# Performance work log

Measured on AMD Instinct MI355X. Metric: run time of the kernel, lower is better.

The kernel has to match this reference:

```python
import jax, jax.numpy as jnp
import numpy as np
from jax import lax

B, T, I, H, O = 64, 1024, 128, 512, 10
TAU_MIN, TAU_MAX = 5.0, 50.0


def setup_inputs() -> dict:
    key = jax.random.key(0)
    ks = jax.random.split(key, 12)
    s = lambda fan_in: 1.0 / np.sqrt(fan_in)
    x = jax.random.normal(ks[0], (B, T, I), dtype=jnp.float32)
    W_in = jax.random.normal(ks[1], (I, H), dtype=jnp.float32) * s(I)
    b_in = jnp.zeros((H,), dtype=jnp.float32)
    # recurrent weight, scaled down to mimic spectral-radius 0.9 init
    W_rec = jax.random.normal(ks[2], (H, H), dtype=jnp.float32) * (0.9 / np.sqrt(H))
    bias = jnp.zeros((H,), dtype=jnp.float32)
    W_tau1 = jax.random.normal(ks[3], (2 * H, H // 2), dtype=jnp.float32) * s(2 * H)
    b_tau1 = jnp.zeros((H // 2,), dtype=jnp.float32)
    W_tau2 = jax.random.normal(ks[4], (H // 2, H), dtype=jnp.float32) * s(H // 2)
    b_tau2 = jnp.zeros((H,), dtype=jnp.float32)
    W_out = jax.random.normal(ks[5], (H, O), dtype=jnp.float32) * s(H)
    b_out = jnp.zeros((O,), dtype=jnp.float32)
    return {"x": x, "W_in": W_in, "b_in": b_in, "W_rec": W_rec, "bias": bias,
            "W_tau1": W_tau1, "b_tau1": b_tau1, "W_tau2": W_tau2, "b_tau2": b_tau2,
            "W_out": W_out, "b_out": b_out}


def reference(x, W_in, b_in, W_rec, bias, W_tau1, b_tau1, W_tau2, b_tau2, W_out, b_out):
    # Input projection precomputed for all timesteps: [B, T, H]
    xp = jnp.einsum('bti,ih->bth', x, W_in) + b_in

    def step(h, xt):
        # tau adapter MLP: sigmoid(relu(cat(x,h) W1 + b1) W2 + b2)
        ctx = jnp.concatenate([xt, h], axis=-1)          # [B, 2H]
        tau_scale = jax.nn.sigmoid(jax.nn.relu(ctx @ W_tau1 + b_tau1) @ W_tau2 + b_tau2)
        tau = TAU_MIN + tau_scale * (TAU_MAX - TAU_MIN)  # [B, H]
        drive = jnp.tanh(xt + h @ W_rec.T + bias)
        new_h = h + (-h + drive) / tau                   # Euler step, dt = 1
        return new_h, new_h

    h0 = jnp.zeros((x.shape[0], W_rec.shape[0]), dtype=x.dtype)
    _, hs = lax.scan(step, h0, jnp.swapaxes(xp, 0, 1))   # [T, B, H]
    hs = jnp.swapaxes(hs, 0, 1)                          # [B, T, H]
    return hs @ W_out + b_out                            # [B, T, O]
```

## Files before the change

### kernel.cpp

```cpp
#include <hip/hip_runtime.h>
#include <hip/hip_fp16.h>
#include <math.h>

#define Bsz 64
#define Tsz 1024
#define Isz 128
#define Hsz 512
#define KH  256
#define Osz 10

__global__ __launch_bounds__(256) void gemm_bias_kernel(
    const float* __restrict__ A, const float* __restrict__ Bw,
    const float* __restrict__ bias, float* __restrict__ C,
    int M, int N, int K)
{
  __shared__ float As[32][68];
  const int tid = threadIdx.x;
  const int m0 = blockIdx.x * 64;
  const int n0 = blockIdx.y * 128;
  const int ty = tid >> 5, tx = tid & 31;

  float acc[8][4] = {{0.f}};

  for (int kk = 0; kk < K; kk += 32) {
    __syncthreads();
#pragma unroll
    for (int i = tid; i < 64 * 32; i += 256) {
      int m = i >> 5, k = i & 31;
      As[k][m] = A[(size_t)(m0 + m) * K + kk + k];
    }
    __syncthreads();
#pragma unroll
    for (int k = 0; k < 32; ++k) {
      const float4 bv = *(const float4*)(&Bw[(size_t)(kk + k) * N + n0 + tx * 4]);
      float a[8];
#pragma unroll
      for (int i = 0; i < 8; ++i) a[i] = As[k][ty * 8 + i];
#pragma unroll
      for (int i = 0; i < 8; ++i) {
        acc[i][0] = fmaf(a[i], bv.x, acc[i][0]);
        acc[i][1] = fmaf(a[i], bv.y, acc[i][1]);
        acc[i][2] = fmaf(a[i], bv.z, acc[i][2]);
        acc[i][3] = fmaf(a[i], bv.w, acc[i][3]);
      }
    }
  }

  const float4 bb = *(const float4*)(&bias[n0 + tx * 4]);
#pragma unroll
  for (int i = 0; i < 8; ++i) {
    float4 v;
    v.x = acc[i][0] + bb.x; v.y = acc[i][1] + bb.y;
    v.z = acc[i][2] + bb.z; v.w = acc[i][3] + bb.w;
    *(float4*)(&C[(size_t)(m0 + ty * 8 + i) * N + n0 + tx * 4]) = v;
  }
}

__global__ __launch_bounds__(256) void wc_kernel(
    const float* __restrict__ W_in, const float* __restrict__ W1a,
    float* __restrict__ Wc)
{
  __shared__ float row[Hsz];
  const int i = blockIdx.x, c = threadIdx.x;
  for (int h = c; h < Hsz; h += 256) row[h] = W_in[(size_t)i * Hsz + h];
  __syncthreads();
  float acc = 0.f;
#pragma unroll 8
  for (int h = 0; h < Hsz; ++h)
    acc = fmaf(row[h], W1a[(size_t)h * KH + c], acc);
  Wc[(size_t)i * KH + c] = acc;
}

__global__ __launch_bounds__(256) void bu_kernel(
    const float* __restrict__ b_in, const float* __restrict__ W1a,
    const float* __restrict__ b_tau1, float* __restrict__ bU)
{
  const int c = threadIdx.x;
  float acc = b_tau1[c];
#pragma unroll 8
  for (int h = 0; h < Hsz; ++h)
    acc = fmaf(b_in[h], W1a[(size_t)h * KH + c], acc);
  bU[c] = acc;
}

__device__ __forceinline__ int dot4i8(int a, int b, int acc) {
#if __has_builtin(__builtin_amdgcn_sdot4)
  return __builtin_amdgcn_sdot4(a, b, acc, false);
#else
  acc += ((a << 24) >> 24) * ((b << 24) >> 24);
  acc += ((a << 16) >> 24) * ((b << 16) >> 24);
  acc += ((a << 8)  >> 24) * ((b << 8)  >> 24);
  acc += (a >> 24) * (b >> 24);
  return acc;
#endif
}


__global__ __launch_bounds__(256) void drive_scale_kernel(
    const float* __restrict__ W_rec, float* __restrict__ CS0)
{
  const int j = blockIdx.x * 256 + threadIdx.x;
  float m = 0.f;
  for (int k = 0; k < Hsz; ++k)
    m = fmaxf(m, fabsf(W_rec[(size_t)j * Hsz + k]));
  CS0[j] = m;
}

__global__ __launch_bounds__(256) void drive_quant_kernel(
    const float* __restrict__ W_rec, const float* __restrict__ CS0,
    unsigned* __restrict__ Q0)
{
  int i = blockIdx.x * 256 + threadIdx.x;
  if (i >= 32 * Hsz * 4) return;
  int di = i & 3, j = (i >> 2) & 511, g = i >> 11;
  int k0 = 16 * g + 4 * di;
  float ma = CS0[j];
  float r = (ma > 0.f) ? (127.f / ma) : 0.f;
  unsigned out = 0;
#pragma unroll
  for (int e = 0; e < 4; ++e) {
    int q = __float2int_rn(W_rec[(size_t)j * Hsz + k0 + e] * r);
    out |= ((unsigned)(q & 255)) << (8 * e);
  }
  Q0[i] = out;
}

__global__ __launch_bounds__(256) void tau1_scale_kernel(
    const float* __restrict__ W1b, float* __restrict__ CS1)
{
  const int c = threadIdx.x;
  float m = 0.f;
  for (int j = 0; j < Hsz; ++j)
    m = fmaxf(m, fabsf(W1b[(size_t)j * KH + c]));
  CS1[c] = m;
}

__global__ __launch_bounds__(256) void tau1_quant_kernel(
    const float* __restrict__ W1b, const float* __restrict__ CS1,
    unsigned* __restrict__ Q1)
{
  int i = blockIdx.x * 256 + threadIdx.x;
  if (i >= 32 * KH * 4) return;
  int di = i & 3, c = (i >> 2) & 255, g = i >> 10;
  int j0 = 16 * g + 4 * di;
  float ma = CS1[c];
  float r = (ma > 0.f) ? (127.f / ma) : 0.f;
  unsigned out = 0;
#pragma unroll
  for (int e = 0; e < 4; ++e) {
    int q = __float2int_rn(W1b[(size_t)(j0 + e) * KH + c] * r);
    out |= ((unsigned)(q & 255)) << (8 * e);
  }
  Q1[i] = out;
}

__global__ __launch_bounds__(256) void tau2_scale_kernel(
    const float* __restrict__ W_tau2, float* __restrict__ CS2)
{
  const int j = blockIdx.x * 256 + threadIdx.x;
  float m = 0.f;
  for (int k = 0; k < KH; ++k)
    m = fmaxf(m, fabsf(W_tau2[(size_t)k * Hsz + j]));
  CS2[j] = m;
}

__global__ __launch_bounds__(256) void tau2_quant_kernel(
    const float* __restrict__ W_tau2, const float* __restrict__ CS2,
    unsigned* __restrict__ Q2)
{
  int i = blockIdx.x * 256 + threadIdx.x;
  if (i >= 16 * Hsz * 4) return;
  int di = i & 3, j = (i >> 2) & 511, g = i >> 11;
  int k0 = 16 * g + 4 * di;
  float ma = CS2[j];
  float r = (ma > 0.f) ? (127.f / ma) : 0.f;
  unsigned out = 0;
#pragma unroll
  for (int e = 0; e < 4; ++e) {
    int q = __float2int_rn(W_tau2[(size_t)(k0 + e) * Hsz + j] * r);
    out |= ((unsigned)(q & 255)) << (8 * e);
  }
  Q2[i] = out;
}

__global__ __launch_bounds__(512) void scan_kernel(
    float* __restrict__ xps,
    const float* __restrict__ U,
    const unsigned* __restrict__ Q0,
    const unsigned* __restrict__ Q1,
    const unsigned* __restrict__ Q2,
    const float* __restrict__ CS0,
    const float* __restrict__ CS1,
    const float* __restrict__ CS2,
    const float* __restrict__ bias,
    const float* __restrict__ b_tau2)
{
  const int b = blockIdx.x;
  const int tid = threadIdx.x;
  const int hs = tid >> 8;
  const int c  = tid & 255;

  extern __shared__ __align__(16) uint4 Wlds[];
  __shared__ __align__(16) int Hq[2][128];
  __shared__ __align__(16) unsigned char Aq[KH];
  __shared__ float scaleA[4];
  __shared__ int parti[2][KH];

  const float bias_r = bias[tid];
  const float bt2_r  = b_tau2[tid];
  const float cs0r = CS0[tid] * (1.0f / 16129.0f);
  const float csr  = CS1[c]   * (1.0f / 16129.0f);
  const float cs2r = CS2[tid] * (1.0f / 16129.0f);
  float hold = 0.f;
  if (tid < 128) { Hq[0][tid] = 0; Hq[1][tid] = 0; }

  float* xprow = xps + (size_t)b * Tsz * Hsz;
  const float* Urow = U + (size_t)b * Tsz * KH;

  const uint4* __restrict__ q0 = (const uint4*)Q0 + tid;
  const uint4* __restrict__ q1 = (const uint4*)Q1 + (size_t)(hs * 16) * 256 + c;
  const uint4* __restrict__ q2 = (const uint4*)Q2 + tid;
  const uint4* Aq4 = (const uint4*)Aq;

#pragma unroll
  for (int i = 0; i < 16; ++i)
    Wlds[i * 512 + tid] = q2[(size_t)i * 512];
#pragma unroll
  for (int i = 0; i < 2; ++i)
    Wlds[8192 + i * 512 + tid] = q0[(size_t)(30 + i) * 512];

  uint4 w0r[28];
#pragma unroll
  for (int g = 0; g < 28; ++g) w0r[g] = q0[(size_t)g * 512];
  uint4 w1r[16];
#pragma unroll
  for (int g = 0; g < 16; ++g) w1r[g] = q1[(size_t)g * 256];

  __syncthreads();

  float xpv = xprow[tid];
  float Uv  = (tid < KH) ? Urow[tid] : 0.f;

  for (int t = 0; t < Tsz; ++t) {
    const uint4* h4 = (const uint4*)Hq[t & 1];

    int a0 = 0, a1 = 0;
#pragma unroll
    for (int g = 0; g < 16; ++g) {
      const uint4 w  = w1r[g];
      const uint4 hv = h4[hs * 16 + g];
      a0 = dot4i8((int)w.x, (int)hv.x, a0); a1 = dot4i8((int)w.y, (int)hv.y, a1);
      a0 = dot4i8((int)w.z, (int)hv.z, a0); a1 = dot4i8((int)w.w, (int)hv.w, a1);
    }
    parti[hs][c] = a0 + a1;
    __syncthreads();

    if (tid < KH) {
      float aval = fmaxf(Uv + (float)(parti[0][tid] + parti[1][tid]) * csr, 0.f);
      float m = aval;
#pragma unroll
      for (int off = 32; off >= 1; off >>= 1)
        m = fmaxf(m, __shfl_xor(m, off));
      if ((tid & 63) == 0) scaleA[tid >> 6] = m;
      const float r = (m > 0.f) ? (127.f / m) : 0.f;
      Aq[tid] = (unsigned char)__float2int_rn(aval * r);
    }
    __syncthreads();

    const float xpn = xprow[Hsz + tid];
    const float Un  = (tid < KH) ? Urow[KH + tid] : 0.f;

    int d0i = 0, d1i = 0;
    int t2a0 = 0, t2a1 = 0;
    float s = bt2_r;
#pragma unroll
    for (int g = 0; g < 16; ++g) {
      uint4 w0, w1;
      if (g < 14) {
        w0 = w0r[2 * g];
        w1 = w0r[2 * g + 1];
      } else if (g == 14) {
        w0 = q0[(size_t)28 * 512];
        w1 = q0[(size_t)29 * 512];
      } else {
        w0 = Wlds[8192 + tid];
        w1 = Wlds[8192 + 512 + tid];
      }
      const uint4 hv0 = h4[2 * g], hv1 = h4[2 * g + 1];
      d0i = dot4i8((int)w0.x, (int)hv0.x, d0i); d1i = dot4i8((int)w0.y, (int)hv0.y, d1i);
      d0i = dot4i8((int)w0.z, (int)hv0.z, d0i); d1i = dot4i8((int)w0.w, (int)hv0.w, d1i);
      d0i = dot4i8((int)w1.x, (int)hv1.x, d0i); d1i = dot4i8((int)w1.y, (int)hv1.y, d1i);
      d0i = dot4i8((int)w1.z, (int)hv1.z, d0i); d1i = dot4i8((int)w1.w, (int)hv1.w, d1i);

      const uint4 wt = Wlds[g * 512 + tid];
      const uint4 av = Aq4[g];
      t2a0 = dot4i8((int)wt.x, (int)av.x, t2a0); t2a1 = dot4i8((int)wt.y, (int)av.y, t2a1);
      t2a0 = dot4i8((int)wt.z, (int)av.z, t2a0); t2a1 = dot4i8((int)wt.w, (int)av.w, t2a1);
      if ((g & 3) == 3) {
        s += (float)(t2a0 + t2a1) * cs2r * scaleA[g >> 2];
        t2a0 = 0; t2a1 = 0;
      }
    }

    const float d = xpv + bias_r + (float)(d0i + d1i) * cs0r;
    const float tau = 5.0f + 45.0f / (1.0f + __expf(-s));
    const float e2 = __expf(2.0f * d);
    const float drv = 1.0f - 2.0f / (e2 + 1.0f);
    const float hnew = hold + (drv - hold) / tau;
    hold = hnew;
    ((char*)Hq[(t + 1) & 1])[tid] = (char)(__float2int_rn(hnew * 127.f) & 255);
    xprow[tid] = hnew;
    __syncthreads();

    xpv = xpn; Uv = Un;
    xprow += Hsz;
    Urow  += KH;
  }
}

__global__ __launch_bounds__(256) void outproj_kernel(
    const float* __restrict__ hs, const float* __restrict__ W_out,
    const float* __restrict__ b_out, float* __restrict__ out)
{
  __shared__ float hsL[16][516];
  __shared__ float WL[Hsz * Osz];
  const int tid = threadIdx.x;
  const size_t m0 = (size_t)blockIdx.x * 16;

  for (int i = tid; i < Hsz * Osz; i += 256) WL[i] = W_out[i];

  const float4* src = (const float4*)(hs + m0 * Hsz);
#pragma unroll
  for (int i = 0; i < 8; ++i) {
    int idx = i * 256 + tid;
    *(float4*)&hsL[idx >> 7][(idx & 127) * 4] = src[idx];
  }
  __syncthreads();

  const int r = tid >> 4, o = tid & 15;
  if (o < Osz) {
    float acc = b_out[o];
#pragma unroll 8
    for (int k4 = 0; k4 < 128; ++k4) {
      const float4 h4 = *(const float4*)&hsL[r][k4 * 4];
      acc = fmaf(h4.x, WL[(4 * k4 + 0) * Osz + o], acc);
      acc = fmaf(h4.y, WL[(4 * k4 + 1) * Osz + o], acc);
      acc = fmaf(h4.z, WL[(4 * k4 + 2) * Osz + o], acc);
      acc = fmaf(h4.w, WL[(4 * k4 + 3) * Osz + o], acc);
    }
    out[(m0 + r) * Osz + o] = acc;
  }
}

extern "C" void kernel_launch(void* const* d_in, const int* in_sizes, int n_in,
                              void* d_out, int out_size, void* d_ws, size_t ws_size,
                              hipStream_t stream) {
  (void)in_sizes; (void)n_in; (void)out_size; (void)ws_size;

  const float* x      = (const float*)d_in[0];
  const float* W_in   = (const float*)d_in[1];
  const float* b_in   = (const float*)d_in[2];
  const float* W_rec  = (const float*)d_in[3];
  const float* bias   = (const float*)d_in[4];
  const float* W_tau1 = (const float*)d_in[5];
  const float* b_tau1 = (const float*)d_in[6];
  const float* W_tau2 = (const float*)d_in[7];
  const float* b_tau2 = (const float*)d_in[8];
  const float* W_out  = (const float*)d_in[9];
  const float* b_out  = (const float*)d_in[10];
  float* out = (float*)d_out;

  char* ws = (char*)d_ws;
  size_t off = 0;
  float* xps = (float*)(ws + off); off += (size_t)Bsz * Tsz * Hsz * 4;
  float* U   = (float*)(ws + off); off += (size_t)Bsz * Tsz * KH * 4;
  unsigned* Q0 = (unsigned*)(ws + off); off += (size_t)32 * Hsz * 4 * 4;
  unsigned* Q1 = (unsigned*)(ws + off); off += (size_t)32 * KH  * 4 * 4;
  unsigned* Q2 = (unsigned*)(ws + off); off += (size_t)16 * Hsz * 4 * 4;
  float* CS0   = (float*)(ws + off); off += 512 * 4;
  float* CS1   = (float*)(ws + off); off += 256 * 4;
  float* CS2   = (float*)(ws + off); off += 512 * 4;
  float* Wc    = (float*)(ws + off); off += (size_t)Isz * KH * 4;
  float* bU    = (float*)(ws + off); off += 256 * 4;

  const float* W1a = W_tau1;
  const float* W1b = W_tau1 + (size_t)Hsz * KH;

  const int M = Bsz * Tsz;

  (void)hipFuncSetAttribute((const void*)scan_kernel,
                            hipFuncAttributeMaxDynamicSharedMemorySize, 147456);

  drive_scale_kernel<<<2, 256, 0, stream>>>(W_rec, CS0);
  drive_quant_kernel<<<256, 256, 0, stream>>>(W_rec, CS0, Q0);
  tau1_scale_kernel<<<1, 256, 0, stream>>>(W1b, CS1);
  tau1_quant_kernel<<<128, 256, 0, stream>>>(W1b, CS1, Q1);
  tau2_scale_kernel<<<2, 256, 0, stream>>>(W_tau2, CS2);
  tau2_quant_kernel<<<128, 256, 0, stream>>>(W_tau2, CS2, Q2);
  wc_kernel<<<Isz, 256, 0, stream>>>(W_in, W1a, Wc);
  bu_kernel<<<1, 256, 0, stream>>>(b_in, W1a, b_tau1, bU);

  {
    dim3 grid(M / 64, Hsz / 128);
    gemm_bias_kernel<<<grid, 256, 0, stream>>>(x, W_in, b_in, xps, M, Hsz, Isz);
  }
  {
    dim3 grid(M / 64, KH / 128);
    gemm_bias_kernel<<<grid, 256, 0, stream>>>(x, Wc, bU, U, M, KH, Isz);
  }
  scan_kernel<<<Bsz, 512, 147456, stream>>>(xps, U, Q0, Q1, Q2,
                                            CS0, CS1, CS2, bias, b_tau2);
  outproj_kernel<<<M / 16, 256, 0, stream>>>(xps, W_out, b_out, out);
}
```

Before: 2.924 ms.

## Split scan recurrence K dimension across two thread halves with 1024-thread blocks

The scan kernel now runs 1024 threads per batch block. Each hidden unit's drive and tau2 dot products are split over two K halves, and the halves combine through shared-memory partials plus an extra barrier per timestep. Per-thread register weight storage drops (12+8 uint4 instead of 28+16), and asm keep-alive constraints hold the weights in registers. The aim is to shorten the serial per-step critical path by doubling parallelism, at the cost of one more __syncthreads per step and lower register budget per thread.

```diff
diff --git a/kernel.cpp b/kernel.cpp
--- a/kernel.cpp
+++ b/kernel.cpp
@@ -183,7 +183,9 @@
   Q2[i] = out;
 }
 
-__global__ __launch_bounds__(512) void scan_kernel(
+#define KEEP4(v) asm volatile("" : "+v"((v).x), "+v"((v).y), "+v"((v).z), "+v"((v).w))
+
+__global__ __launch_bounds__(1024) void scan_kernel(
     float* __restrict__ xps,
     const float* __restrict__ U,
     const unsigned* __restrict__ Q0,
@@ -195,68 +197,85 @@
     const float* __restrict__ bias,
     const float* __restrict__ b_tau2)
 {
-  const int b = blockIdx.x;
+  const int b   = blockIdx.x;
   const int tid = threadIdx.x;
-  const int hs = tid >> 8;
-  const int c  = tid & 255;
+  const int kh  = tid >> 9;
+  const int j   = tid & 511;
+  const int q   = (tid >> 8) & 3;
+  const int c   = tid & 255;
 
   extern __shared__ __align__(16) uint4 Wlds[];
   __shared__ __align__(16) int Hq[2][128];
   __shared__ __align__(16) unsigned char Aq[KH];
   __shared__ float scaleA[4];
-  __shared__ int parti[2][KH];
-
-  const float bias_r = bias[tid];
-  const float bt2_r  = b_tau2[tid];
-  const float cs0r = CS0[tid] * (1.0f / 16129.0f);
-  const float csr  = CS1[c]   * (1.0f / 16129.0f);
-  const float cs2r = CS2[tid] * (1.0f / 16129.0f);
+  __shared__ int   parti[4][KH];
+  __shared__ int   dpart[Hsz];
+  __shared__ float tpart[Hsz];
+
+  const float bias_r = bias[j];
+  const float bt2_r  = b_tau2[j];
+  const float cs0r = CS0[j] * (1.0f / 16129.0f);
+  const float csr  = CS1[c] * (1.0f / 16129.0f);
+  const float cs2r = CS2[j] * (1.0f / 16129.0f);
   float hold = 0.f;
   if (tid < 128) { Hq[0][tid] = 0; Hq[1][tid] = 0; }
 
   float* xprow = xps + (size_t)b * Tsz * Hsz;
   const float* Urow = U + (size_t)b * Tsz * KH;
 
-  const uint4* __restrict__ q0 = (const uint4*)Q0 + tid;
-  const uint4* __restrict__ q1 = (const uint4*)Q1 + (size_t)(hs * 16) * 256 + c;
-  const uint4* __restrict__ q2 = (const uint4*)Q2 + tid;
+  const uint4* __restrict__ Q0u4 = (const uint4*)Q0;
+  const uint4* __restrict__ Q1u4 = (const uint4*)Q1;
+  const uint4* __restrict__ Q2u4 = (const uint4*)Q2;
   const uint4* Aq4 = (const uint4*)Aq;
-
-#pragma unroll
-  for (int i = 0; i < 16; ++i)
-    Wlds[i * 512 + tid] = q2[(size_t)i * 512];
-#pragma unroll
-  for (int i = 0; i < 2; ++i)
-    Wlds[8192 + i * 512 + tid] = q0[(size_t)(30 + i) * 512];
-
-  uint4 w0r[28];
-#pragma unroll
-  for (int g = 0; g < 28; ++g) w0r[g] = q0[(size_t)g * 512];
-  uint4 w1r[16];
-#pragma unroll
-  for (int g = 0; g < 16; ++g) w1r[g] = q1[(size_t)g * 256];
+  const int kh16 = kh * 16, kh8 = kh * 8, kh2 = kh * 2, q8 = q * 8;
+
+#pragma unroll
+  for (int i = 0; i < 8; ++i)
+    Wlds[i * 1024 + tid] = Q2u4[i * 1024 + tid];
+  Wlds[8192 + tid] = Q0u4[(tid < 512) ? (15 * 512 + tid)
+                                      : (31 * 512 + (tid - 512))];
+
+  uint4 w1r[8];
+#pragma unroll
+  for (int gg = 0; gg < 8; ++gg)
+    w1r[gg] = Q1u4[(size_t)(q8 + gg) * 256 + c];
+  uint4 w0r[12];
+#pragma unroll
+  for (int gg = 0; gg < 12; ++gg)
+    w0r[gg] = Q0u4[(size_t)(kh16 + gg) * 512 + j];
+#pragma unroll
+  for (int gg = 0; gg < 8; ++gg) KEEP4(w1r[gg]);
+#pragma unroll
+  for (int gg = 0; gg < 12; ++gg) KEEP4(w0r[gg]);
+
+  const uint4* __restrict__ q0s = Q0u4 + (size_t)(kh16 + 12) * 512 + j;
 
   __syncthreads();
 
-  float xpv = xprow[tid];
+  float xpv = (kh == 0) ? xprow[j] : 0.f;
   float Uv  = (tid < KH) ? Urow[tid] : 0.f;
 
   for (int t = 0; t < Tsz; ++t) {
     const uint4* h4 = (const uint4*)Hq[t & 1];
 
-    int a0 = 0, a1 = 0;
-#pragma unroll
-    for (int g = 0; g < 16; ++g) {
-      const uint4 w  = w1r[g];
-      const uint4 hv = h4[hs * 16 + g];
-      a0 = dot4i8((int)w.x, (int)hv.x, a0); a1 = dot4i8((int)w.y, (int)hv.y, a1);
-      a0 = dot4i8((int)w.z, (int)hv.z, a0); a1 = dot4i8((int)w.w, (int)hv.w, a1);
-    }
-    parti[hs][c] = a0 + a1;
+    const uint4 sA = q0s[0];
+    const uint4 sB = q0s[512];
+    const uint4 sC = q0s[1024];
+
+    int a = 0;
+#pragma unroll
+    for (int gg = 0; gg < 8; ++gg) {
+      const uint4 w  = w1r[gg];
+      const uint4 hv = h4[q8 + gg];
+      a = dot4i8((int)w.x, (int)hv.x, a); a = dot4i8((int)w.y, (int)hv.y, a);
+      a = dot4i8((int)w.z, (int)hv.z, a); a = dot4i8((int)w.w, (int)hv.w, a);
+    }
+    parti[q][c] = a;
     __syncthreads();
 
     if (tid < KH) {
-      float aval = fmaxf(Uv + (float)(parti[0][tid] + parti[1][tid]) * csr, 0.f);
+      float aval = fmaxf(Uv + (float)(parti[0][tid] + parti[1][tid] +
+                                      parti[2][tid] + parti[3][tid]) * csr, 0.f);
       float m = aval;
 #pragma unroll
       for (int off = 32; off >= 1; off >>= 1)
@@ -267,49 +286,66 @@
     }
     __syncthreads();
 
-    const float xpn = xprow[Hsz + tid];
+    const float xpn = (kh == 0) ? xprow[Hsz + j] : 0.f;
     const float Un  = (tid < KH) ? Urow[KH + tid] : 0.f;
-
-    int d0i = 0, d1i = 0;
-    int t2a0 = 0, t2a1 = 0;
-    float s = bt2_r;
-#pragma unroll
-    for (int g = 0; g < 16; ++g) {
-      uint4 w0, w1;
-      if (g < 14) {
-        w0 = w0r[2 * g];
-        w1 = w0r[2 * g + 1];
-      } else if (g == 14) {
-        w0 = q0[(size_t)28 * 512];
-        w1 = q0[(size_t)29 * 512];
-      } else {
-        w0 = Wlds[8192 + tid];
-        w1 = Wlds[8192 + 512 + tid];
+    const float sc0 = scaleA[kh2], sc1 = scaleA[kh2 + 1];
+
+    int d = 0;
+#pragma unroll
+    for (int gg = 0; gg < 12; ++gg) {
+      const uint4 w  = w0r[gg];
+      const uint4 hv = h4[kh16 + gg];
+      d = dot4i8((int)w.x, (int)hv.x, d); d = dot4i8((int)w.y, (int)hv.y, d);
+      d = dot4i8((int)w.z, (int)hv.z, d); d = dot4i8((int)w.w, (int)hv.w, d);
+    }
+    {
+      const uint4 hv = h4[kh16 + 12];
+      d = dot4i8((int)sA.x, (int)hv.x, d); d = dot4i8((int)sA.y, (int)hv.y, d);
+      d = dot4i8((int)sA.z, (int)hv.z, d); d = dot4i8((int)sA.w, (int)hv.w, d);
+    }
+    {
+      const uint4 hv = h4[kh16 + 13];
+      d = dot4i8((int)sB.x, (int)hv.x, d); d = dot4i8((int)sB.y, (int)hv.y, d);
+      d = dot4i8((int)sB.z, (int)hv.z, d); d = dot4i8((int)sB.w, (int)hv.w, d);
+    }
+    {
+      const uint4 hv = h4[kh16 + 14];
+      d = dot4i8((int)sC.x, (int)hv.x, d); d = dot4i8((int)sC.y, (int)hv.y, d);
+      d = dot4i8((int)sC.z, (int)hv.z, d); d = dot4i8((int)sC.w, (int)hv.w, d);
+    }
+    {
+      const uint4 w  = Wlds[8192 + tid];
+      const uint4 hv = h4[kh16 + 15];
+      d = dot4i8((int)w.x, (int)hv.x, d); d = dot4i8((int)w.y, (int)hv.y, d);
+      d = dot4i8((int)w.z, (int)hv.z, d); d = dot4i8((int)w.w, (int)hv.w, d);
+    }
+
+    int t2 = 0; float sp = 0.f;
+#pragma unroll
+    for (int gg = 0; gg < 8; ++gg) {
+      const uint4 wt = Wlds[(kh8 + gg) * 512 + j];
+      const uint4 av = Aq4[kh8 + gg];
+      t2 = dot4i8((int)wt.x, (int)av.x, t2); t2 = dot4i8((int)wt.y, (int)av.y, t2);
+      t2 = dot4i8((int)wt.z, (int)av.z, t2); t2 = dot4i8((int)wt.w, (int)av.w, t2);
+      if ((gg & 3) == 3) {
+        sp += (float)t2 * cs2r * ((gg < 4) ? sc0 : sc1);
+        t2 = 0;
       }
-      const uint4 hv0 = h4[2 * g], hv1 = h4[2 * g + 1];
-      d0i = dot4i8((int)w0.x, (int)hv0.x, d0i); d1i = dot4i8((int)w0.y, (int)hv0.y, d1i);
-      d0i = dot4i8((int)w0.z, (int)hv0.z, d0i); d1i = dot4i8((int)w0.w, (int)hv0.w, d1i);
-      d0i = dot4i8((int)w1.x, (int)hv1.x, d0i); d1i = dot4i8((int)w1.y, (int)hv1.y, d1i);
-      d0i = dot4i8((int)w1.z, (int)hv1.z, d0i); d1i = dot4i8((int)w1.w, (int)hv1.w, d1i);
-
-      const uint4 wt = Wlds[g * 512 + tid];
-      const uint4 av = Aq4[g];
-      t2a0 = dot4i8((int)wt.x, (int)av.x, t2a0); t2a1 = dot4i8((int)wt.y, (int)av.y, t2a1);
-      t2a0 = dot4i8((int)wt.z, (int)av.z, t2a0); t2a1 = dot4i8((int)wt.w, (int)av.w, t2a1);
-      if ((g & 3) == 3) {
-        s += (float)(t2a0 + t2a1) * cs2r * scaleA[g >> 2];
-        t2a0 = 0; t2a1 = 0;
-      }
-    }
-
-    const float d = xpv + bias_r + (float)(d0i + d1i) * cs0r;
-    const float tau = 5.0f + 45.0f / (1.0f + __expf(-s));
-    const float e2 = __expf(2.0f * d);
-    const float drv = 1.0f - 2.0f / (e2 + 1.0f);
-    const float hnew = hold + (drv - hold) / tau;
-    hold = hnew;
-    ((char*)Hq[(t + 1) & 1])[tid] = (char)(__float2int_rn(hnew * 127.f) & 255);
-    xprow[tid] = hnew;
+    }
+    if (kh) { dpart[j] = d; tpart[j] = sp; }
+    __syncthreads();
+
+    if (kh == 0) {
+      const float s  = sp + tpart[j] + bt2_r;
+      const float dd = xpv + bias_r + (float)(d + dpart[j]) * cs0r;
+      const float tau = 5.0f + 45.0f / (1.0f + __expf(-s));
+      const float e2 = __expf(2.0f * dd);
+      const float drv = 1.0f - 2.0f / (e2 + 1.0f);
+      const float hnew = hold + (drv - hold) / tau;
+      hold = hnew;
+      ((char*)Hq[(t + 1) & 1])[j] = (char)(__float2int_rn(hnew * 127.f) & 255);
+      xprow[j] = hnew;
+    }
     __syncthreads();
 
     xpv = xpn; Uv = Un;
@@ -408,7 +444,7 @@
     dim3 grid(M / 64, KH / 128);
     gemm_bias_kernel<<<grid, 256, 0, stream>>>(x, Wc, bU, U, M, KH, Isz);
   }
-  scan_kernel<<<Bsz, 512, 147456, stream>>>(xps, U, Q0, Q1, Q2,
-                                            CS0, CS1, CS2, bias, b_tau2);
+  scan_kernel<<<Bsz, 1024, 147456, stream>>>(xps, U, Q0, Q1, Q2,
+                                             CS0, CS1, CS2, bias, b_tau2);
   outproj_kernel<<<M / 16, 256, 0, stream>>>(xps, W_out, b_out, out);
 }
```

After: 5.606 ms. 91.7% more time.

## Keep scan weights in AGPRs and move one more W_rec slice to LDS

Applied to the files above, without the earlier changes.

Holds most of the int8 recurrent-weight slices and part of the tau1 weights in accumulation registers through inline v_accvgpr_write/read, and moves three W_rec slices into LDS, leaving only one slice fetched from global memory each step. The point is to stop per-timestep global loads and register spills in the serial scan loop. It also interleaves the tau2 dot products between groups of drive dot products and splits the int8 accumulators into four chains to get more instruction-level parallelism. In exchange it adds AGPR read traffic and uses more LDS, and the hand-written asm may limit how the compiler schedules the loop.

```diff
diff --git a/kernel.cpp b/kernel.cpp
--- a/kernel.cpp
+++ b/kernel.cpp
@@ -182,6 +182,11 @@
   }
   Q2[i] = out;
 }
+
+#define AGW(k, x) asm volatile("v_accvgpr_write_b32 %0, %1" : "=a"(ag[k]) : "v"(x))
+#define AGR(k, x) asm volatile("v_accvgpr_read_b32 %0, %1" : "=v"(x) : "a"(ag[k]))
+
+#define KEEP4(v) asm volatile("" : "+v"((v).x), "+v"((v).y), "+v"((v).z), "+v"((v).w))
 
 __global__ __launch_bounds__(512) void scan_kernel(
     float* __restrict__ xps,
@@ -199,6 +204,7 @@
   const int tid = threadIdx.x;
   const int hs = tid >> 8;
   const int c  = tid & 255;
+  const int hs16 = hs * 16;
 
   extern __shared__ __align__(16) uint4 Wlds[];
   __shared__ __align__(16) int Hq[2][128];
@@ -226,17 +232,59 @@
   for (int i = 0; i < 16; ++i)
     Wlds[i * 512 + tid] = q2[(size_t)i * 512];
 #pragma unroll
-  for (int i = 0; i < 2; ++i)
-    Wlds[8192 + i * 512 + tid] = q0[(size_t)(30 + i) * 512];
-
-  uint4 w0r[28];
-#pragma unroll
-  for (int g = 0; g < 28; ++g) w0r[g] = q0[(size_t)g * 512];
-  uint4 w1r[16];
-#pragma unroll
-  for (int g = 0; g < 16; ++g) w1r[g] = q1[(size_t)g * 256];
+  for (int i = 0; i < 3; ++i)
+    Wlds[8192 + i * 512 + tid] = q0[(size_t)(28 + i) * 512];
+
+  unsigned ag[128];
+#pragma unroll
+  for (int g = 0; g < 28; ++g) {
+    const uint4 tw = q0[(size_t)g * 512];
+    AGW(4 * g + 0, tw.x); AGW(4 * g + 1, tw.y);
+    AGW(4 * g + 2, tw.z); AGW(4 * g + 3, tw.w);
+  }
+#pragma unroll
+  for (int g = 0; g < 4; ++g) {
+    const uint4 tw = q1[(size_t)(12 + g) * 256];
+    AGW(112 + 4 * g + 0, tw.x); AGW(112 + 4 * g + 1, tw.y);
+    AGW(112 + 4 * g + 2, tw.z); AGW(112 + 4 * g + 3, tw.w);
+  }
+
+  uint4 w1r[12];
+#pragma unroll
+  for (int g = 0; g < 12; ++g) w1r[g] = q1[(size_t)g * 256];
+#pragma unroll
+  for (int g = 0; g < 12; ++g) KEEP4(w1r[g]);
 
   __syncthreads();
+
+#define DRV_G(g) do { \
+    unsigned wx_, wy_, wz_, ww_; \
+    AGR(4*(g)+0, wx_); AGR(4*(g)+1, wy_); AGR(4*(g)+2, wz_); AGR(4*(g)+3, ww_); \
+    const uint4 hv_ = h4[g]; \
+    dA = dot4i8((int)wx_, (int)hv_.x, dA); dB = dot4i8((int)wy_, (int)hv_.y, dB); \
+    dC = dot4i8((int)wz_, (int)hv_.z, dC); dD = dot4i8((int)ww_, (int)hv_.w, dD); \
+  } while(0)
+
+#define T1_G(g) do { \
+    unsigned wx_, wy_, wz_, ww_; \
+    AGR(112+4*((g)-12)+0, wx_); AGR(112+4*((g)-12)+1, wy_); \
+    AGR(112+4*((g)-12)+2, wz_); AGR(112+4*((g)-12)+3, ww_); \
+    const uint4 hv_ = h4[hs16 + (g)]; \
+    t1a = dot4i8((int)wx_, (int)hv_.x, t1a); t1b = dot4i8((int)wy_, (int)hv_.y, t1b); \
+    t1c = dot4i8((int)wz_, (int)hv_.z, t1c); t1d = dot4i8((int)ww_, (int)hv_.w, t1d); \
+  } while(0)
+
+#define TAU2x4(k) do { \
+    int t2a = 0, t2b = 0, t2c = 0, t2d = 0; \
+    _Pragma("unroll") \
+    for (int g = 4*(k); g < 4*(k) + 4; ++g) { \
+      const uint4 wt = Wlds[g * 512 + tid]; \
+      const uint4 av = Aq4[g]; \
+      t2a = dot4i8((int)wt.x, (int)av.x, t2a); t2b = dot4i8((int)wt.y, (int)av.y, t2b); \
+      t2c = dot4i8((int)wt.z, (int)av.z, t2c); t2d = dot4i8((int)wt.w, (int)av.w, t2d); \
+    } \
+    s += (float)(t2a + t2b + t2c + t2d) * cs2r * scaleA[k]; \
+  } while(0)
 
   float xpv = xprow[tid];
   float Uv  = (tid < KH) ? Urow[tid] : 0.f;
@@ -244,15 +292,18 @@
   for (int t = 0; t < Tsz; ++t) {
     const uint4* h4 = (const uint4*)Hq[t & 1];
 
-    int a0 = 0, a1 = 0;
-#pragma unroll
-    for (int g = 0; g < 16; ++g) {
+    const uint4 s31 = q0[(size_t)31 * 512];
+
+    int t1a = 0, t1b = 0, t1c = 0, t1d = 0;
+#pragma unroll
+    for (int g = 0; g < 12; ++g) {
       const uint4 w  = w1r[g];
-      const uint4 hv = h4[hs * 16 + g];
-      a0 = dot4i8((int)w.x, (int)hv.x, a0); a1 = dot4i8((int)w.y, (int)hv.y, a1);
-      a0 = dot4i8((int)w.z, (int)hv.z, a0); a1 = dot4i8((int)w.w, (int)hv.w, a1);
-    }
-    parti[hs][c] = a0 + a1;
+      const uint4 hv = h4[hs16 + g];
+      t1a = dot4i8((int)w.x, (int)hv.x, t1a); t1b = dot4i8((int)w.y, (int)hv.y, t1b);
+      t1c = dot4i8((int)w.z, (int)hv.z, t1c); t1d = dot4i8((int)w.w, (int)hv.w, t1d);
+    }
+    T1_G(12); T1_G(13); T1_G(14); T1_G(15);
+    parti[hs][c] = t1a + t1b + t1c + t1d;
     __syncthreads();
 
     if (tid < KH) {
@@ -270,39 +321,32 @@
     const float xpn = xprow[Hsz + tid];
     const float Un  = (tid < KH) ? Urow[KH + tid] : 0.f;
 
-    int d0i = 0, d1i = 0;
-    int t2a0 = 0, t2a1 = 0;
+    int dA = 0, dB = 0, dC = 0, dD = 0;
     float s = bt2_r;
-#pragma unroll
-    for (int g = 0; g < 16; ++g) {
-      uint4 w0, w1;
-      if (g < 14) {
-        w0 = w0r[2 * g];
-        w1 = w0r[2 * g + 1];
-      } else if (g == 14) {
-        w0 = q0[(size_t)28 * 512];
-        w1 = q0[(size_t)29 * 512];
-      } else {
-        w0 = Wlds[8192 + tid];
-        w1 = Wlds[8192 + 512 + tid];
-      }
-      const uint4 hv0 = h4[2 * g], hv1 = h4[2 * g + 1];
-      d0i = dot4i8((int)w0.x, (int)hv0.x, d0i); d1i = dot4i8((int)w0.y, (int)hv0.y, d1i);
-      d0i = dot4i8((int)w0.z, (int)hv0.z, d0i); d1i = dot4i8((int)w0.w, (int)hv0.w, d1i);
-      d0i = dot4i8((int)w1.x, (int)hv1.x, d0i); d1i = dot4i8((int)w1.y, (int)hv1.y, d1i);
-      d0i = dot4i8((int)w1.z, (int)hv1.z, d0i); d1i = dot4i8((int)w1.w, (int)hv1.w, d1i);
-
-      const uint4 wt = Wlds[g * 512 + tid];
-      const uint4 av = Aq4[g];
-      t2a0 = dot4i8((int)wt.x, (int)av.x, t2a0); t2a1 = dot4i8((int)wt.y, (int)av.y, t2a1);
-      t2a0 = dot4i8((int)wt.z, (int)av.z, t2a0); t2a1 = dot4i8((int)wt.w, (int)av.w, t2a1);
-      if ((g & 3) == 3) {
-        s += (float)(t2a0 + t2a1) * cs2r * scaleA[g >> 2];
-        t2a0 = 0; t2a1 = 0;
-      }
-    }
-
-    const float d = xpv + bias_r + (float)(d0i + d1i) * cs0r;
+
+    DRV_G(0);  DRV_G(1);  DRV_G(2);  DRV_G(3);  DRV_G(4);  DRV_G(5);  DRV_G(6);
+    TAU2x4(0);
+    DRV_G(7);  DRV_G(8);  DRV_G(9);  DRV_G(10); DRV_G(11); DRV_G(12); DRV_G(13);
+    TAU2x4(1);
+    DRV_G(14); DRV_G(15); DRV_G(16); DRV_G(17); DRV_G(18); DRV_G(19); DRV_G(20);
+    TAU2x4(2);
+    DRV_G(21); DRV_G(22); DRV_G(23); DRV_G(24); DRV_G(25); DRV_G(26); DRV_G(27);
+    TAU2x4(3);
+
+#pragma unroll
+    for (int i = 0; i < 3; ++i) {
+      const uint4 w  = Wlds[8192 + i * 512 + tid];
+      const uint4 hv = h4[28 + i];
+      dA = dot4i8((int)w.x, (int)hv.x, dA); dB = dot4i8((int)w.y, (int)hv.y, dB);
+      dC = dot4i8((int)w.z, (int)hv.z, dC); dD = dot4i8((int)w.w, (int)hv.w, dD);
+    }
+    {
+      const uint4 hv = h4[31];
+      dA = dot4i8((int)s31.x, (int)hv.x, dA); dB = dot4i8((int)s31.y, (int)hv.y, dB);
+      dC = dot4i8((int)s31.z, (int)hv.z, dC); dD = dot4i8((int)s31.w, (int)hv.w, dD);
+    }
+
+    const float d = xpv + bias_r + (float)(dA + dB + dC + dD) * cs0r;
     const float tau = 5.0f + 45.0f / (1.0f + __expf(-s));
     const float e2 = __expf(2.0f * d);
     const float drv = 1.0f - 2.0f / (e2 + 1.0f);
@@ -316,6 +360,9 @@
     xprow += Hsz;
     Urow  += KH;
   }
+#undef DRV_G
+#undef T1_G
+#undef TAU2x4
 }
 
 __global__ __launch_bounds__(256) void outproj_kernel(
@@ -389,7 +436,7 @@
   const int M = Bsz * Tsz;
 
   (void)hipFuncSetAttribute((const void*)scan_kernel,
-                            hipFuncAttributeMaxDynamicSharedMemorySize, 147456);
+                            hipFuncAttributeMaxDynamicSharedMemorySize, 155648);
 
   drive_scale_kernel<<<2, 256, 0, stream>>>(W_rec, CS0);
   drive_quant_kernel<<<256, 256, 0, stream>>>(W_rec, CS0, Q0);
@@ -408,7 +455,7 @@
     dim3 grid(M / 64, KH / 128);
     gemm_bias_kernel<<<grid, 256, 0, stream>>>(x, Wc, bU, U, M, KH, Isz);
   }
-  scan_kernel<<<Bsz, 512, 147456, stream>>>(xps, U, Q0, Q1, Q2,
+  scan_kernel<<<Bsz, 512, 155648, stream>>>(xps, U, Q0, Q1, Q2,
                                             CS0, CS1, CS2, bias, b_tau2);
   outproj_kernel<<<M / 16, 256, 0, stream>>>(xps, W_out, b_out, out);
 }
```

New measurement: 6.184 ms. +111.5%, slower.

## Stream W_rec int8 weights from global/L2 instead of registers in scan

Applied to the files above, without the earlier changes.

The scan kernel stops holding 28 uint4 W_rec weight fragments in registers. It now reloads most of them from global memory (expected to hit L2/L1) every timestep, issuing the first four loads early so they overlap the tau1 phase. One more weight slice moves into LDS, so dynamic shared memory grows to 155648 bytes, and asm volatile keeps the w1r fragments pinned in registers. The aim is to cut register pressure or spilling in the serial recurrence, at the cost of repeated per-step memory traffic on the critical path.

```diff
diff --git a/kernel.cpp b/kernel.cpp
--- a/kernel.cpp
+++ b/kernel.cpp
@@ -182,6 +182,8 @@
   }
   Q2[i] = out;
 }
+
+#define KEEP4(v) asm volatile("" : "+v"((v).x), "+v"((v).y), "+v"((v).z), "+v"((v).w))
 
 __global__ __launch_bounds__(512) void scan_kernel(
     float* __restrict__ xps,
@@ -199,6 +201,7 @@
   const int tid = threadIdx.x;
   const int hs = tid >> 8;
   const int c  = tid & 255;
+  const int hs16 = hs * 16;
 
   extern __shared__ __align__(16) uint4 Wlds[];
   __shared__ __align__(16) int Hq[2][128];
@@ -226,15 +229,14 @@
   for (int i = 0; i < 16; ++i)
     Wlds[i * 512 + tid] = q2[(size_t)i * 512];
 #pragma unroll
-  for (int i = 0; i < 2; ++i)
-    Wlds[8192 + i * 512 + tid] = q0[(size_t)(30 + i) * 512];
-
-  uint4 w0r[28];
-#pragma unroll
-  for (int g = 0; g < 28; ++g) w0r[g] = q0[(size_t)g * 512];
+  for (int i = 0; i < 3; ++i)
+    Wlds[8192 + i * 512 + tid] = q0[(size_t)(28 + i) * 512];
+
   uint4 w1r[16];
 #pragma unroll
   for (int g = 0; g < 16; ++g) w1r[g] = q1[(size_t)g * 256];
+#pragma unroll
+  for (int g = 0; g < 16; ++g) KEEP4(w1r[g]);
 
   __syncthreads();
 
@@ -244,15 +246,20 @@
   for (int t = 0; t < Tsz; ++t) {
     const uint4* h4 = (const uint4*)Hq[t & 1];
 
-    int a0 = 0, a1 = 0;
+    const uint4 s0 = q0[(size_t)0 * 512];
+    const uint4 s1 = q0[(size_t)1 * 512];
+    const uint4 s2 = q0[(size_t)2 * 512];
+    const uint4 s3 = q0[(size_t)3 * 512];
+
+    int t1a = 0, t1b = 0;
 #pragma unroll
     for (int g = 0; g < 16; ++g) {
       const uint4 w  = w1r[g];
-      const uint4 hv = h4[hs * 16 + g];
-      a0 = dot4i8((int)w.x, (int)hv.x, a0); a1 = dot4i8((int)w.y, (int)hv.y, a1);
-      a0 = dot4i8((int)w.z, (int)hv.z, a0); a1 = dot4i8((int)w.w, (int)hv.w, a1);
-    }
-    parti[hs][c] = a0 + a1;
+      const uint4 hv = h4[hs16 + g];
+      t1a = dot4i8((int)w.x, (int)hv.x, t1a); t1b = dot4i8((int)w.y, (int)hv.y, t1b);
+      t1a = dot4i8((int)w.z, (int)hv.z, t1a); t1b = dot4i8((int)w.w, (int)hv.w, t1b);
+    }
+    parti[hs][c] = t1a + t1b;
     __syncthreads();
 
     if (tid < KH) {
@@ -270,39 +277,41 @@
     const float xpn = xprow[Hsz + tid];
     const float Un  = (tid < KH) ? Urow[KH + tid] : 0.f;
 
-    int d0i = 0, d1i = 0;
-    int t2a0 = 0, t2a1 = 0;
+    int dA = 0, dB = 0;
+    int t2a = 0, t2b = 0;
     float s = bt2_r;
 #pragma unroll
-    for (int g = 0; g < 16; ++g) {
+    for (int gg = 0; gg < 16; ++gg) {
       uint4 w0, w1;
-      if (g < 14) {
-        w0 = w0r[2 * g];
-        w1 = w0r[2 * g + 1];
-      } else if (g == 14) {
-        w0 = q0[(size_t)28 * 512];
-        w1 = q0[(size_t)29 * 512];
-      } else {
+      if (gg == 0)      { w0 = s0; w1 = s1; }
+      else if (gg == 1) { w0 = s2; w1 = s3; }
+      else if (gg < 14) {
+        w0 = q0[(size_t)(2 * gg) * 512];
+        w1 = q0[(size_t)(2 * gg + 1) * 512];
+      } else if (gg == 14) {
         w0 = Wlds[8192 + tid];
         w1 = Wlds[8192 + 512 + tid];
+      } else {
+        w0 = Wlds[8192 + 1024 + tid];
+        w1 = q0[(size_t)31 * 512];
       }
-      const uint4 hv0 = h4[2 * g], hv1 = h4[2 * g + 1];
-      d0i = dot4i8((int)w0.x, (int)hv0.x, d0i); d1i = dot4i8((int)w0.y, (int)hv0.y, d1i);
-      d0i = dot4i8((int)w0.z, (int)hv0.z, d0i); d1i = dot4i8((int)w0.w, (int)hv0.w, d1i);
-      d0i = dot4i8((int)w1.x, (int)hv1.x, d0i); d1i = dot4i8((int)w1.y, (int)hv1.y, d1i);
-      d0i = dot4i8((int)w1.z, (int)hv1.z, d0i); d1i = dot4i8((int)w1.w, (int)hv1.w, d1i);
-
-      const uint4 wt = Wlds[g * 512 + tid];
-      const uint4 av = Aq4[g];
-      t2a0 = dot4i8((int)wt.x, (int)av.x, t2a0); t2a1 = dot4i8((int)wt.y, (int)av.y, t2a1);
-      t2a0 = dot4i8((int)wt.z, (int)av.z, t2a0); t2a1 = dot4i8((int)wt.w, (int)av.w, t2a1);
-      if ((g & 3) == 3) {
-        s += (float)(t2a0 + t2a1) * cs2r * scaleA[g >> 2];
-        t2a0 = 0; t2a1 = 0;
+      const uint4 hv0 = h4[2 * gg], hv1 = h4[2 * gg + 1];
+      dA = dot4i8((int)w0.x, (int)hv0.x, dA); dB = dot4i8((int)w0.y, (int)hv0.y, dB);
+      dA = dot4i8((int)w0.z, (int)hv0.z, dA); dB = dot4i8((int)w0.w, (int)hv0.w, dB);
+      dA = dot4i8((int)w1.x, (int)hv1.x, dA); dB = dot4i8((int)w1.y, (int)hv1.y, dB);
+      dA = dot4i8((int)w1.z, (int)hv1.z, dA); dB = dot4i8((int)w1.w, (int)hv1.w, dB);
+
+      const uint4 wt = Wlds[gg * 512 + tid];
+      const uint4 av = Aq4[gg];
+      t2a = dot4i8((int)wt.x, (int)av.x, t2a); t2b = dot4i8((int)wt.y, (int)av.y, t2b);
+      t2a = dot4i8((int)wt.z, (int)av.z, t2a); t2b = dot4i8((int)wt.w, (int)av.w, t2b);
+      if ((gg & 3) == 3) {
+        s += (float)(t2a + t2b) * cs2r * scaleA[gg >> 2];
+        t2a = 0; t2b = 0;
       }
     }
 
-    const float d = xpv + bias_r + (float)(d0i + d1i) * cs0r;
+    const float d = xpv + bias_r + (float)(dA + dB) * cs0r;
     const float tau = 5.0f + 45.0f / (1.0f + __expf(-s));
     const float e2 = __expf(2.0f * d);
     const float drv = 1.0f - 2.0f / (e2 + 1.0f);
@@ -389,7 +398,7 @@
   const int M = Bsz * Tsz;
 
   (void)hipFuncSetAttribute((const void*)scan_kernel,
-                            hipFuncAttributeMaxDynamicSharedMemorySize, 147456);
+                            hipFuncAttributeMaxDynamicSharedMemorySize, 155648);
 
   drive_scale_kernel<<<2, 256, 0, stream>>>(W_rec, CS0);
   drive_quant_kernel<<<256, 256, 0, stream>>>(W_rec, CS0, Q0);
@@ -408,7 +417,7 @@
     dim3 grid(M / 64, KH / 128);
     gemm_bias_kernel<<<grid, 256, 0, stream>>>(x, Wc, bU, U, M, KH, Isz);
   }
-  scan_kernel<<<Bsz, 512, 147456, stream>>>(xps, U, Q0, Q1, Q2,
+  scan_kernel<<<Bsz, 512, 155648, stream>>>(xps, U, Q0, Q1, Q2,
                                             CS0, CS1, CS2, bias, b_tau2);
   outproj_kernel<<<M / 16, 256, 0, stream>>>(xps, W_out, b_out, out);
 }
```

Result: no change. 2.927 ms (+0.1%).
